# Kernel optimization log

Measured on AMD Instinct MI355X. Metric: run time of the kernel, lower is better.

Reference implementation:

```python
import jax, jax.numpy as jnp
import numpy as np

THETA = 10000.0
R_TOK = 4  # region_token_num


def _local_positions(regions, max_n):
    # 0-based position of each token within its region (count of prior tokens
    # with the same region id) -- order-based, works for any region layout.
    onehot = jax.nn.one_hot(regions, max_n + 1, dtype=jnp.int32)  # [B,T,N+1]
    counts = jnp.cumsum(onehot, axis=1)                            # inclusive
    return jnp.take_along_axis(counts, regions[..., None], axis=-1)[..., 0] - 1


def _rope(q, k, pos, theta):
    # full-head-dim rotary embedding, split-half convention
    D = q.shape[-1]
    inv_freq = 1.0 / (theta ** (jnp.arange(0, D, 2, dtype=jnp.float32) / D))  # [D/2]
    ang = pos[..., None].astype(jnp.float32) * inv_freq                        # [B,S,D/2]
    cos = jnp.tile(jnp.cos(ang), (1, 1, 2))[:, None]                           # [B,1,S,D]
    sin = jnp.tile(jnp.sin(ang), (1, 1, 2))[:, None]

    def rot(x):
        h = x.shape[-1] // 2
        return jnp.concatenate([-x[..., h:], x[..., :h]], axis=-1)

    return q * cos + rot(q) * sin, k * cos + rot(k) * sin


def setup_inputs() -> dict:
    B, H, D = 2, 16, 64
    T, MAX_N = 2048, 64
    P = MAX_N * R_TOK
    key = jax.random.key(0)
    ks = jax.random.split(key, 7)
    f = lambda k, s: jax.random.normal(k, s, dtype=jnp.float32)
    regions = jnp.sort(jax.random.randint(ks[6], (B, T), 1, MAX_N + 1, dtype=jnp.int32), axis=-1)
    return {
        'pool_q': f(ks[0], (B, H, P, D)),
        'pool_k': f(ks[1], (B, H, P, D)),
        'pool_v': f(ks[2], (B, H, P, D)),
        'x_q': f(ks[3], (B, H, T, D)),
        'x_k': f(ks[4], (B, H, T, D)),
        'x_v': f(ks[5], (B, H, T, D)),
        'regions': regions,
        't_mask': jnp.ones((B, T), dtype=bool),
        'n_mask': jnp.ones((B, MAX_N), dtype=bool),
        'max_n': MAX_N,
    }


def reference(pool_q, pool_k, pool_v, x_q, x_k, x_v, regions, t_mask, n_mask, max_n):
    B, H, P, D = pool_q.shape
    R = R_TOK
    # sequence = [pool, x]
    q = jnp.concatenate([pool_q, x_q], axis=2)
    k = jnp.concatenate([pool_k, x_k], axis=2)
    v = jnp.concatenate([pool_v, x_v], axis=2)

    # local-mode positions (use_pool_offset=False -> pool tokens at pos 0)
    pool_pos = jnp.zeros((B, P), dtype=jnp.int32)
    x_pos = (_local_positions(regions, max_n) + R) * (regions > 0).astype(jnp.int32)
    pos = jnp.concatenate([pool_pos, x_pos], axis=-1)  # [B,S]
    q, k = _rope(q, k, pos, THETA)

    # block-local (same-region) mask: [B,1,S,S], True = allowed
    pool_region = jnp.broadcast_to(jnp.repeat(jnp.arange(1, max_n + 1, dtype=jnp.int32), R)[None], (B, P))
    pool_valid = jnp.repeat(n_mask, R, axis=1)                      # [B,P]
    full_region = jnp.concatenate([pool_region, regions], axis=-1)  # [B,S]
    full_valid = jnp.concatenate([pool_valid, t_mask], axis=-1)     # [B,S]
    same = full_region[:, :, None] == full_region[:, None, :]
    valid = full_valid[:, :, None] & full_valid[:, None, :]
    nonpad = (full_region != 0)[:, :, None] & (full_region != 0)[:, None, :]
    mask = (same & valid & nonpad)[:, None]                          # [B,1,S,S]

    scores = jnp.einsum('bhqd,bhkd->bhqk', q, k) / jnp.sqrt(jnp.float32(D))
    scores = jnp.where(mask, scores, jnp.float32(-1e9))
    attn = jax.nn.softmax(scores, axis=-1)
    out = jnp.einsum('bhqk,bhkd->bhqd', attn, v)
    return out[:, :, :P, :]
```

## Files before the change

### kernel.cpp

```cpp
#include <hip/hip_runtime.h>
#include <hip/hip_bf16.h>

#define BB   2
#define HH   16
#define DD   64
#define TT   2048
#define MAXN 64
#define RTOK 4
#define PP   (MAXN * RTOK)

__global__ __launch_bounds__(256, 8)
void lapd_attn(const float* __restrict__ pool_q,
               const float* __restrict__ pool_k,
               const float* __restrict__ pool_v,
               const float* __restrict__ x_k,
               const float* __restrict__ x_v,
               const int* __restrict__ regions,
               float* __restrict__ out) {
    const int blk   = blockIdx.x;
    const int r_idx = blk & (MAXN - 1);
    const int bh    = blk >> 6;
    const int r     = r_idx + 1;
    const int b     = bh / HH;

    const int tid  = threadIdx.x;
    const int wave = tid >> 6;
    const int lane = tid & 63;

    __shared__ float k_s[64][DD + 1];
    __shared__ float q_s[4][DD];
    __shared__ float p_s[4][64];
    __shared__ int   cnt_s[4];

    {
        const int4* reg4 = (const int4*)(regions + b * TT);
        int c_lt = 0, c_le = 0;
        #pragma unroll
        for (int i = 0; i < 2; ++i) {
            const int4 v = reg4[tid + i * 256];
            c_lt += (v.x <  r) + (v.y <  r) + (v.z <  r) + (v.w <  r);
            c_le += (v.x <= r) + (v.y <= r) + (v.z <= r) + (v.w <= r);
        }
        int packed = c_lt | (c_le << 16);
        #pragma unroll
        for (int off = 32; off > 0; off >>= 1)
            packed += __shfl_xor(packed, off, 64);
        if (lane == 0) cnt_s[wave] = packed;
    }
    __syncthreads();
    const int tot    = cnt_s[0] + cnt_s[1] + cnt_s[2] + cnt_s[3];
    const int start  = tot & 0xFFFF;
    const int n_keys = ((tot >> 16) & 0xFFFF) - start + RTOK;

    const size_t poolbase = ((size_t)bh * PP + r_idx * RTOK) * DD;
    const float* pk = pool_k + poolbase;
    const float* pv = pool_v + poolbase;
    const float* xk = x_k + (size_t)bh * TT * DD;
    const float* xv = x_v + (size_t)bh * TT * DD;

    q_s[wave][lane] = pool_q[poolbase + (size_t)(wave * DD) + lane] * 0.125f;

    float m = -1e30f, l = 0.0f, acc = 0.0f;

    for (int tile = 0; tile < n_keys; tile += 64) {
        const int tn = min(64, n_keys - tile);
        __syncthreads();
        for (int base = 0; base < tn * DD; base += 1024) {
            const int flat = base + tid * 4;
            if (flat < tn * DD) {
                const int key = flat >> 6;
                const int dim = flat & 63;
                const int gk  = tile + key;
                float kr[4];
                if (gk < RTOK) {
                    const float4 kv = *(const float4*)(pk + gk * DD + dim);
                    kr[0] = kv.x; kr[1] = kv.y; kr[2] = kv.z; kr[3] = kv.w;
                } else {
                    const size_t off = (size_t)(start + gk - RTOK) * DD;
                    const float4 kv = *(const float4*)(xk + off + dim);
                    const float4 kp = *(const float4*)(xk + off + ((dim + 32) & 63));
                    const float pos = (float)gk;
                    const float sgn = (dim < 32) ? -1.0f : 1.0f;
                    const float kd[4]  = {kv.x, kv.y, kv.z, kv.w};
                    const float kpd[4] = {kp.x, kp.y, kp.z, kp.w};
                    #pragma unroll
                    for (int c = 0; c < 4; ++c) {
                        const int j = (dim + c) & 31;
                        const float invf = __expf((float)j * (-9.210340371976184f / 32.0f));
                        float sv, cv;
                        __sincosf(pos * invf, &sv, &cv);
                        kr[c] = kd[c] * cv + sgn * kpd[c] * sv;
                    }
                }
                k_s[key][dim + 0] = kr[0];
                k_s[key][dim + 1] = kr[1];
                k_s[key][dim + 2] = kr[2];
                k_s[key][dim + 3] = kr[3];
            }
        }
        __syncthreads();

        float s = -1e30f;
        if (lane < tn) {
            float s0 = 0, s1 = 0, s2 = 0, s3 = 0;
            #pragma unroll
            for (int d = 0; d < DD; d += 4) {
                s0 += q_s[wave][d + 0] * k_s[lane][d + 0];
                s1 += q_s[wave][d + 1] * k_s[lane][d + 1];
                s2 += q_s[wave][d + 2] * k_s[lane][d + 2];
                s3 += q_s[wave][d + 3] * k_s[lane][d + 3];
            }
            s = (s0 + s1) + (s2 + s3);
        }
        float tm = s;
        #pragma unroll
        for (int off = 32; off > 0; off >>= 1)
            tm = fmaxf(tm, __shfl_xor(tm, off, 64));
        const float m_new = fmaxf(m, tm);
        const float alpha = __expf(m - m_new);
        const float p = (lane < tn) ? __expf(s - m_new) : 0.0f;
        float ts = p;
        #pragma unroll
        for (int off = 32; off > 0; off >>= 1)
            ts += __shfl_xor(ts, off, 64);
        l = l * alpha + ts;
        m = m_new;
        p_s[wave][lane] = p;

        acc *= alpha;
        int k = 0;
        if (tile == 0) {
            #pragma unroll
            for (int kk = 0; kk < RTOK; ++kk)
                acc += p_s[wave][kk] * pv[kk * DD + lane];
            k = RTOK;
        }
        float a0 = 0, a1 = 0, a2 = 0, a3 = 0;
        for (; k + 3 < tn; k += 4) {
            const size_t o = (size_t)(start + tile + k - RTOK) * DD + lane;
            a0 += p_s[wave][k + 0] * xv[o];
            a1 += p_s[wave][k + 1] * xv[o + DD];
            a2 += p_s[wave][k + 2] * xv[o + 2 * DD];
            a3 += p_s[wave][k + 3] * xv[o + 3 * DD];
        }
        for (; k < tn; ++k)
            acc += p_s[wave][k] * xv[(size_t)(start + tile + k - RTOK) * DD + lane];
        acc += (a0 + a1) + (a2 + a3);
    }

    out[poolbase + (size_t)(wave * DD) + lane] = acc / l;
}

extern "C" void kernel_launch(void* const* d_in, const int* in_sizes, int n_in,
                              void* d_out, int out_size, void* d_ws, size_t ws_size,
                              hipStream_t stream) {
    const float* pool_q  = (const float*)d_in[0];
    const float* pool_k  = (const float*)d_in[1];
    const float* pool_v  = (const float*)d_in[2];
    const float* x_k     = (const float*)d_in[4];
    const float* x_v     = (const float*)d_in[5];
    const int*   regions = (const int*)d_in[6];
    float*       out     = (float*)d_out;

    lapd_attn<<<dim3(BB * HH * MAXN), dim3(256), 0, stream>>>(
        pool_q, pool_k, pool_v, x_k, x_v, regions, out);
}
```

Before: 121.6 us.

## Stage V tiles in shared memory with batched K/V loads before RoPE

V rows are now loaded cooperatively into a padded shared-memory tile alongside K, instead of each of the four waves re-reading V from global memory in the PV loop. All K/V global loads for a tile are issued up front into registers before the RoPE math, so their latencies overlap. The pool_q load is also hoisted ahead of the region-count reduction. In exchange, LDS use doubles and launch bounds drop to 4 blocks per CU, which lowers occupancy and raises register pressure from the buffered float4 arrays.

Measured after the change: 119.6 us. No clear change (-1.6%).

```diff
diff --git a/kernel.cpp b/kernel.cpp
--- a/kernel.cpp
+++ b/kernel.cpp
@@ -8,8 +8,9 @@
 #define MAXN 64
 #define RTOK 4
 #define PP   (MAXN * RTOK)
+#define KPAD 65
 
-__global__ __launch_bounds__(256, 8)
+__global__ __launch_bounds__(256, 4)
 void lapd_attn(const float* __restrict__ pool_q,
                const float* __restrict__ pool_k,
                const float* __restrict__ pool_v,
@@ -27,10 +28,21 @@
     const int wave = tid >> 6;
     const int lane = tid & 63;
 
-    __shared__ float k_s[64][DD + 1];
+    __shared__ float k_s[64][KPAD];
+    __shared__ float v_s[64][KPAD];
     __shared__ float q_s[4][DD];
     __shared__ float p_s[4][64];
     __shared__ int   cnt_s[4];
+
+    const size_t poolbase = ((size_t)bh * PP + r_idx * RTOK) * DD;
+    const float* pk = pool_k + poolbase;
+    const float* pv = pool_v + poolbase;
+    const float* xk = x_k + (size_t)bh * TT * DD;
+    const float* xv = x_v + (size_t)bh * TT * DD;
+
+    const size_t qidx = poolbase + (size_t)(wave * DD) + lane;
+    const float qv = pool_q[qidx] * 0.125f;
+    q_s[wave][lane] = qv;
 
     {
         const int4* reg4 = (const int4*)(regions + b * TT);
@@ -52,50 +64,61 @@
     const int start  = tot & 0xFFFF;
     const int n_keys = ((tot >> 16) & 0xFFFF) - start + RTOK;
 
-    const size_t poolbase = ((size_t)bh * PP + r_idx * RTOK) * DD;
-    const float* pk = pool_k + poolbase;
-    const float* pv = pool_v + poolbase;
-    const float* xk = x_k + (size_t)bh * TT * DD;
-    const float* xv = x_v + (size_t)bh * TT * DD;
-
-    q_s[wave][lane] = pool_q[poolbase + (size_t)(wave * DD) + lane] * 0.125f;
-
     float m = -1e30f, l = 0.0f, acc = 0.0f;
 
     for (int tile = 0; tile < n_keys; tile += 64) {
         const int tn = min(64, n_keys - tile);
         __syncthreads();
-        for (int base = 0; base < tn * DD; base += 1024) {
-            const int flat = base + tid * 4;
+
+        float4 kvb[4], kpb[4], vvb[4];
+        #pragma unroll
+        for (int p = 0; p < 4; ++p) {
+            const int flat = p * 1024 + tid * 4;
             if (flat < tn * DD) {
                 const int key = flat >> 6;
                 const int dim = flat & 63;
                 const int gk  = tile + key;
-                float kr[4];
                 if (gk < RTOK) {
-                    const float4 kv = *(const float4*)(pk + gk * DD + dim);
-                    kr[0] = kv.x; kr[1] = kv.y; kr[2] = kv.z; kr[3] = kv.w;
+                    kvb[p] = *(const float4*)(pk + gk * DD + dim);
+                    kpb[p] = kvb[p];
+                    vvb[p] = *(const float4*)(pv + gk * DD + dim);
                 } else {
                     const size_t off = (size_t)(start + gk - RTOK) * DD;
-                    const float4 kv = *(const float4*)(xk + off + dim);
-                    const float4 kp = *(const float4*)(xk + off + ((dim + 32) & 63));
+                    kvb[p] = *(const float4*)(xk + off + dim);
+                    kpb[p] = *(const float4*)(xk + off + ((dim + 32) & 63));
+                    vvb[p] = *(const float4*)(xv + off + dim);
+                }
+            }
+        }
+        #pragma unroll
+        for (int p = 0; p < 4; ++p) {
+            const int flat = p * 1024 + tid * 4;
+            if (flat < tn * DD) {
+                const int key = flat >> 6;
+                const int dim = flat & 63;
+                const int gk  = tile + key;
+                float kr[4] = {kvb[p].x, kvb[p].y, kvb[p].z, kvb[p].w};
+                if (gk >= RTOK) {
                     const float pos = (float)gk;
                     const float sgn = (dim < 32) ? -1.0f : 1.0f;
-                    const float kd[4]  = {kv.x, kv.y, kv.z, kv.w};
-                    const float kpd[4] = {kp.x, kp.y, kp.z, kp.w};
+                    const float kpd[4] = {kpb[p].x, kpb[p].y, kpb[p].z, kpb[p].w};
                     #pragma unroll
                     for (int c = 0; c < 4; ++c) {
                         const int j = (dim + c) & 31;
                         const float invf = __expf((float)j * (-9.210340371976184f / 32.0f));
                         float sv, cv;
                         __sincosf(pos * invf, &sv, &cv);
-                        kr[c] = kd[c] * cv + sgn * kpd[c] * sv;
+                        kr[c] = kr[c] * cv + sgn * kpd[c] * sv;
                     }
                 }
                 k_s[key][dim + 0] = kr[0];
                 k_s[key][dim + 1] = kr[1];
                 k_s[key][dim + 2] = kr[2];
                 k_s[key][dim + 3] = kr[3];
+                v_s[key][dim + 0] = vvb[p].x;
+                v_s[key][dim + 1] = vvb[p].y;
+                v_s[key][dim + 2] = vvb[p].z;
+                v_s[key][dim + 3] = vvb[p].w;
             }
         }
         __syncthreads();
@@ -128,27 +151,20 @@
         p_s[wave][lane] = p;
 
         acc *= alpha;
+        float a0 = 0, a1 = 0, a2 = 0, a3 = 0;
         int k = 0;
-        if (tile == 0) {
-            #pragma unroll
-            for (int kk = 0; kk < RTOK; ++kk)
-                acc += p_s[wave][kk] * pv[kk * DD + lane];
-            k = RTOK;
-        }
-        float a0 = 0, a1 = 0, a2 = 0, a3 = 0;
         for (; k + 3 < tn; k += 4) {
-            const size_t o = (size_t)(start + tile + k - RTOK) * DD + lane;
-            a0 += p_s[wave][k + 0] * xv[o];
-            a1 += p_s[wave][k + 1] * xv[o + DD];
-            a2 += p_s[wave][k + 2] * xv[o + 2 * DD];
-            a3 += p_s[wave][k + 3] * xv[o + 3 * DD];
+            a0 += p_s[wave][k + 0] * v_s[k + 0][lane];
+            a1 += p_s[wave][k + 1] * v_s[k + 1][lane];
+            a2 += p_s[wave][k + 2] * v_s[k + 2][lane];
+            a3 += p_s[wave][k + 3] * v_s[k + 3][lane];
         }
         for (; k < tn; ++k)
-            acc += p_s[wave][k] * xv[(size_t)(start + tile + k - RTOK) * DD + lane];
+            acc += p_s[wave][k] * v_s[k][lane];
         acc += (a0 + a1) + (a2 + a3);
     }
 
-    out[poolbase + (size_t)(wave * DD) + lane] = acc / l;
+    out[qidx] = acc / l;
 }
 
 extern "C" void kernel_launch(void* const* d_in, const int* in_sizes, int n_in,
```
